# Optimization experiments

Measured on AMD Instinct MI355X. Metric: run time of the kernel, lower is better.

The kernel has to match this reference:

```python
import jax, jax.numpy as jnp
import numpy as np

C0 = 32          # cs[0] == cs[1] with planes=[32,32,...], cr=1.0
CIN = 4
EPS = 1e-5

# ---------- host-side coordinate hashing (mirrors F.sphash / F.sphashquery) ----------

def _enc(c):
    # unique int64 code per (x,y,z); +2 shift keeps offset-adjusted coords positive
    return (c[:, 0] + 2).astype(np.int64) + (c[:, 1] + 2).astype(np.int64) * 1024 \
        + (c[:, 2] + 2).astype(np.int64) * 1024 * 1024

def _lookup(sorted_codes, q):
    pos = np.searchsorted(sorted_codes, q)
    pos = np.minimum(pos, len(sorted_codes) - 1)
    return np.where(sorted_codes[pos] == q, pos, -1).astype(np.int32)

def _offsets(r):
    return np.array([[i, j, k] for i in r for j in r for k in r], np.int64)


def setup_inputs() -> dict:
    rng = np.random.default_rng(0)
    N0 = 400000
    pts = rng.integers(0, [400, 400, 40], size=(600000, 3)).astype(np.int64)
    codes = _enc(pts)
    codes_u, idx = np.unique(codes, return_index=True)
    assert len(codes_u) >= N0
    coords0, codes0 = pts[idx][:N0], codes_u[:N0]   # sorted by hash code

    off27, off8 = _offsets([-1, 0, 1]), _offsets([0, 1])
    # ks=3 stride=1 kernel map at level 0: nbr0[k, i] = index of coords0[i]+off27[k] (or -1)
    nbr0 = np.stack([_lookup(codes0, _enc(coords0 + o)) for o in off27])

    # stride-2 downsample coords (level 1)
    c1all = coords0 // 2
    codes1_u, i1 = np.unique(_enc(c1all), return_index=True)
    coords1 = c1all[i1]
    # ks=2 stride=2 kernel map: output voxel gathers inputs at 2*out + {0,1}^3
    down1 = np.stack([_lookup(codes0, _enc(coords1 * 2 + o)) for o in off8])
    # ks=3 stride=1 kernel map at level 1
    nbr1 = np.stack([_lookup(codes1_u, _enc(coords1 + o)) for o in off27])

    key = jax.random.key(0)
    ks = jax.random.split(key, 10)

    def w(k, K, ci, co):
        return jax.random.normal(k, (K, ci, co), jnp.float32) * (1.0 / np.sqrt(K * ci))

    return {
        "voxel_features": jax.random.normal(ks[0], (N0, CIN), jnp.float32),
        "W_stem1": w(ks[1], 27, CIN, C0),
        "W_stem2": w(ks[2], 27, C0, C0),
        "W_down":  w(ks[3], 8,  C0, C0),
        "W_r1a":   w(ks[4], 27, C0, C0),
        "W_r1b":   w(ks[5], 27, C0, C0),
        "W_r2a":   w(ks[6], 27, C0, C0),
        "W_r2b":   w(ks[7], 27, C0, C0),
        "gammas": jnp.ones((7, C0), jnp.float32),
        "betas":  jnp.zeros((7, C0), jnp.float32),
        "nbr0":  jnp.asarray(nbr0),
        "down1": jnp.asarray(down1),
        "nbr1":  jnp.asarray(nbr1),
    }


# ---------- sparse conv: gather-GEMM-scatter per kernel offset ----------

def _spconv(feat, nbr, W):
    # feat [N, Ci], nbr [K, M] (-1 = no neighbor), W [K, Ci, Co] -> out [M, Co]
    def step(acc, kw):
        idx, Wk = kw
        g = jnp.where((idx >= 0)[:, None], feat[jnp.maximum(idx, 0)], 0.0)
        return acc + g @ Wk, None
    acc0 = jnp.zeros((nbr.shape[1], W.shape[-1]), feat.dtype)
    out, _ = jax.lax.scan(step, acc0, (nbr, W))
    return out


def _bn(x, g, b):
    # BatchNorm1d, training-mode statistics (biased var), gamma/beta affine
    mu = x.mean(0)
    var = x.var(0)
    return (x - mu) * jax.lax.rsqrt(var + EPS) * g + b


def _cbr(x, nbr, W, g, b):
    return jax.nn.relu(_bn(_spconv(x, nbr, W), g, b))


def reference(voxel_features, W_stem1, W_stem2, W_down, W_r1a, W_r1b, W_r2a, W_r2b,
              gammas, betas, nbr0, down1, nbr1):
    g, b = gammas, betas
    # stem: two ks=3 sparse convs + BN + ReLU at level 0
    x = _cbr(voxel_features, nbr0, W_stem1, g[0], b[0])
    x = _cbr(x, nbr0, W_stem2, g[1], b[1])
    # stage1: BasicConvolutionBlock (ks=2, stride=2) + 2 ResidualBlocks at level 1
    x1 = _cbr(x, down1, W_down, g[2], b[2])
    h = _cbr(x1, nbr1, W_r1a, g[3], b[3])
    h = _bn(_spconv(h, nbr1, W_r1b), g[4], b[4])
    x1 = jax.nn.relu(h + x1)          # downsample == Identity (inc == outc, stride 1)
    h = _cbr(x1, nbr1, W_r2a, g[5], b[5])
    h = _bn(_spconv(h, nbr1, W_r2b), g[6], b[6])
    return jax.nn.relu(h + x1)
```

## Files before the change

kernel.cpp:

```cpp
#include <hip/hip_runtime.h>

#define EPS 1e-5f

typedef __attribute__((ext_vector_type(8))) short short8;
typedef __attribute__((ext_vector_type(4))) float floatx4;
typedef __attribute__((ext_vector_type(8))) unsigned short ushort8;
typedef __attribute__((ext_vector_type(4))) unsigned short ushortv4;

#define O_S1  0
#define O_S2  4096
#define O_DN  (O_S2 + 27648)
#define O_R1A (O_DN + 8192)
#define O_R1B (O_R1A + 27648)
#define O_R2A (O_R1B + 27648)
#define O_R2B (O_R2A + 27648)
#define WP_TOTAL (O_R2B + 27648)

__device__ __forceinline__ unsigned short f2bf(float f) {
    union { float f; unsigned u; } x; x.f = f;
    unsigned r = x.u + 0x7fffu + ((x.u >> 16) & 1u);
    return (unsigned short)(r >> 16);
}
__device__ __forceinline__ float bf2f(unsigned short b) {
    union { unsigned u; float f; } x; x.u = ((unsigned)b) << 16;
    return x.f;
}

__device__ __forceinline__ int xcd_swizzle(int nb) {
    int b = (int)blockIdx.x;
    int q = nb >> 3, r = nb & 7;
    int x = b & 7, i = b >> 3;
    return x * q + (x < r ? x : r) + i;
}

__device__ __forceinline__ void pack_w_one(
    const float* __restrict__ W, unsigned short* __restrict__ out, int t)
{
    int lane = t & 63;
    int h = (t >> 6) & 1;
    int k = t >> 7;
    int m = lane & 15, q = lane >> 4;
    ushort8 v;
#pragma unroll
    for (int j = 0; j < 8; ++j)
        v[j] = f2bf(W[((size_t)k * 32 + q * 8 + j) * 32 + h * 16 + m]);
    *(ushort8*)(out + (size_t)t * 8) = v;
}

__global__ __launch_bounds__(256) void prep_kernel(
    const float* __restrict__ vf,
    const float* __restrict__ Ws1, const float* __restrict__ Ws2,
    const float* __restrict__ Wd,  const float* __restrict__ Wr1a,
    const float* __restrict__ Wr1b, const float* __restrict__ Wr2a,
    const float* __restrict__ Wr2b,
    unsigned short* __restrict__ xb, unsigned short* __restrict__ wp, int N0)
{
    int t = blockIdx.x * 256 + threadIdx.x;
    if (t < N0) {
        float4 v = *(const float4*)(vf + (size_t)t * 4);
        ushortv4 r = {f2bf(v.x), f2bf(v.y), f2bf(v.z), f2bf(v.w)};
        *(ushortv4*)(xb + (size_t)t * 4) = r;
        return;
    }
    t -= N0;
    if (t < 512) {
        int lane = t & 63;
        int h = (t >> 6) & 1;
        int c = t >> 7;
        int m = lane & 15, q = lane >> 4;
        ushort8 v;
#pragma unroll
        for (int j = 0; j < 8; ++j) {
            int kdim = c * 32 + q * 8 + j;
            int tap = kdim >> 2, ci = kdim & 3;
            v[j] = (tap < 27) ? f2bf(Ws1[((size_t)tap * 4 + ci) * 32 + h * 16 + m]) : 0;
        }
        *(ushort8*)(wp + O_S1 + (size_t)t * 8) = v;
        return;
    }
    t -= 512;
    if (t < 27 * 128) { pack_w_one(Ws2,  wp + O_S2,  t); return; }
    t -= 27 * 128;
    if (t < 8 * 128)  { pack_w_one(Wd,   wp + O_DN,  t); return; }
    t -= 8 * 128;
    if (t < 27 * 128) { pack_w_one(Wr1a, wp + O_R1A, t); return; }
    t -= 27 * 128;
    if (t < 27 * 128) { pack_w_one(Wr1b, wp + O_R1B, t); return; }
    t -= 27 * 128;
    if (t < 27 * 128) { pack_w_one(Wr2a, wp + O_R2A, t); return; }
    t -= 27 * 128;
    if (t < 27 * 128) { pack_w_one(Wr2b, wp + O_R2B, t); return; }
}

__device__ __forceinline__ void conv_epilogue(
    floatx4 acc00, floatx4 acc01, floatx4 acc10, floatx4 acc11,
    unsigned short* __restrict__ y, float* __restrict__ part,
    int rowbase, int lb, int N, float* sm)
{
    const int lane = threadIdx.x & 63;
    const int m = lane & 15, q = lane >> 4;

    if (threadIdx.x < 64) sm[threadIdx.x] = 0.f;
    __syncthreads();

#pragma unroll
    for (int r = 0; r < 4; ++r) {
        int ra = rowbase + q * 4 + r;
        int rb = ra + 16;
        if (ra < N) {
            y[(size_t)ra * 32 + m]      = f2bf(acc00[r]);
            y[(size_t)ra * 32 + 16 + m] = f2bf(acc01[r]);
        }
        if (rb < N) {
            y[(size_t)rb * 32 + m]      = f2bf(acc10[r]);
            y[(size_t)rb * 32 + 16 + m] = f2bf(acc11[r]);
        }
    }

    float s0 = 0.f, q0 = 0.f, s1 = 0.f, q1 = 0.f;
#pragma unroll
    for (int r = 0; r < 4; ++r) {
        s0 += acc00[r] + acc10[r];
        q0 += acc00[r] * acc00[r] + acc10[r] * acc10[r];
        s1 += acc01[r] + acc11[r];
        q1 += acc01[r] * acc01[r] + acc11[r] * acc11[r];
    }
    s0 += __shfl_down(s0, 32); s0 += __shfl_down(s0, 16);
    q0 += __shfl_down(q0, 32); q0 += __shfl_down(q0, 16);
    s1 += __shfl_down(s1, 32); s1 += __shfl_down(s1, 16);
    q1 += __shfl_down(q1, 32); q1 += __shfl_down(q1, 16);
    if (lane < 16) {
        atomicAdd(&sm[m],      s0);
        atomicAdd(&sm[32 + m], q0);
        atomicAdd(&sm[16 + m],      s1);
        atomicAdd(&sm[48 + m], q1);
    }
    __syncthreads();
    if (threadIdx.x < 64)
        part[(size_t)lb * 64 + threadIdx.x] = sm[threadIdx.x];
}

template <int K>
__global__ __launch_bounds__(256) void conv_mfma_kernel(
    const unsigned short* __restrict__ x,
    const int* __restrict__ nbr,
    const unsigned short* __restrict__ Wp,
    unsigned short* __restrict__ y,
    float* __restrict__ part, int N)
{
    __shared__ float sm[64];
    const int nb = (N + 127) / 128;
    const int lb = xcd_swizzle(nb);
    const int lane = threadIdx.x & 63;
    const int wave = threadIdx.x >> 6;
    const int m = lane & 15, q = lane >> 4;
    const int rowbase = lb * 128 + wave * 32;
    const int row0 = rowbase + m;
    const int row1 = rowbase + 16 + m;

    floatx4 acc00 = {0.f, 0.f, 0.f, 0.f};
    floatx4 acc01 = acc00, acc10 = acc00, acc11 = acc00;

    for (int k = 0; k < K; ++k) {
        int i0 = (row0 < N) ? nbr[(size_t)k * N + row0] : -1;
        int i1 = (row1 < N) ? nbr[(size_t)k * N + row1] : -1;
        short8 a0 = {}, a1 = {};
        if (i0 >= 0) a0 = *(const short8*)(x + (size_t)i0 * 32 + q * 8);
        if (i1 >= 0) a1 = *(const short8*)(x + (size_t)i1 * 32 + q * 8);
        const short8* wk = (const short8*)(Wp + (size_t)k * 2 * 64 * 8);
        short8 b0 = wk[lane];
        short8 b1 = wk[64 + lane];
        acc00 = __builtin_amdgcn_mfma_f32_16x16x32_bf16(a0, b0, acc00, 0, 0, 0);
        acc01 = __builtin_amdgcn_mfma_f32_16x16x32_bf16(a0, b1, acc01, 0, 0, 0);
        acc10 = __builtin_amdgcn_mfma_f32_16x16x32_bf16(a1, b0, acc10, 0, 0, 0);
        acc11 = __builtin_amdgcn_mfma_f32_16x16x32_bf16(a1, b1, acc11, 0, 0, 0);
    }

    conv_epilogue(acc00, acc01, acc10, acc11, y, part, rowbase, lb, N, sm);
}

__global__ __launch_bounds__(256) void conv_stem1_mfma(
    const unsigned short* __restrict__ xb,
    const int* __restrict__ nbr,
    const unsigned short* __restrict__ Wp,
    unsigned short* __restrict__ y,
    float* __restrict__ part, int N)
{
    __shared__ float sm[64];
    const int nb = (N + 127) / 128;
    const int lb = xcd_swizzle(nb);
    const int lane = threadIdx.x & 63;
    const int wave = threadIdx.x >> 6;
    const int m = lane & 15, q = lane >> 4;
    const int rowbase = lb * 128 + wave * 32;
    const int row0 = rowbase + m;
    const int row1 = rowbase + 16 + m;

    floatx4 acc00 = {0.f, 0.f, 0.f, 0.f};
    floatx4 acc01 = acc00, acc10 = acc00, acc11 = acc00;

#pragma unroll
    for (int c = 0; c < 4; ++c) {
        const int t0 = c * 8 + q * 2, t1 = t0 + 1;
        short8 a0 = {}, a1 = {};
        {
            int ia = (t0 < 27 && row0 < N) ? nbr[(size_t)t0 * N + row0] : -1;
            int ib = (t1 < 27 && row0 < N) ? nbr[(size_t)t1 * N + row0] : -1;
            ushortv4 ga = {}, gb = {};
            if (ia >= 0) ga = *(const ushortv4*)(xb + (size_t)ia * 4);
            if (ib >= 0) gb = *(const ushortv4*)(xb + (size_t)ib * 4);
            a0[0] = (short)ga[0]; a0[1] = (short)ga[1];
            a0[2] = (short)ga[2]; a0[3] = (short)ga[3];
            a0[4] = (short)gb[0]; a0[5] = (short)gb[1];
            a0[6] = (short)gb[2]; a0[7] = (short)gb[3];
        }
        {
            int ia = (t0 < 27 && row1 < N) ? nbr[(size_t)t0 * N + row1] : -1;
            int ib = (t1 < 27 && row1 < N) ? nbr[(size_t)t1 * N + row1] : -1;
            ushortv4 ga = {}, gb = {};
            if (ia >= 0) ga = *(const ushortv4*)(xb + (size_t)ia * 4);
            if (ib >= 0) gb = *(const ushortv4*)(xb + (size_t)ib * 4);
            a1[0] = (short)ga[0]; a1[1] = (short)ga[1];
            a1[2] = (short)ga[2]; a1[3] = (short)ga[3];
            a1[4] = (short)gb[0]; a1[5] = (short)gb[1];
            a1[6] = (short)gb[2]; a1[7] = (short)gb[3];
        }
        const short8* wk = (const short8*)Wp;
        short8 b0 = wk[(c * 2 + 0) * 64 + lane];
        short8 b1 = wk[(c * 2 + 1) * 64 + lane];
        acc00 = __builtin_amdgcn_mfma_f32_16x16x32_bf16(a0, b0, acc00, 0, 0, 0);
        acc01 = __builtin_amdgcn_mfma_f32_16x16x32_bf16(a0, b1, acc01, 0, 0, 0);
        acc10 = __builtin_amdgcn_mfma_f32_16x16x32_bf16(a1, b0, acc10, 0, 0, 0);
        acc11 = __builtin_amdgcn_mfma_f32_16x16x32_bf16(a1, b1, acc11, 0, 0, 0);
    }

    conv_epilogue(acc00, acc01, acc10, acc11, y, part, rowbase, lb, N, sm);
}

__global__ __launch_bounds__(256) void reduce_stats_kernel(
    const float* __restrict__ part, float* __restrict__ stats, int nb)
{
    __shared__ float sm[256];
    int t = threadIdx.x;
    int c = t & 63, g = t >> 6;
    float s = 0.f;
    for (int b = blockIdx.x * 4 + g; b < nb; b += 256)
        s += part[(size_t)b * 64 + c];
    sm[t] = s;
    __syncthreads();
    if (t < 64)
        atomicAdd(&stats[t], sm[t] + sm[64 + t] + sm[128 + t] + sm[192 + t]);
}

template <bool OUT_F32, bool HAS_RES>
__global__ __launch_bounds__(256) void bn_relu_kernel(
    const unsigned short* __restrict__ y, const float* __restrict__ stats,
    const float* __restrict__ gamma, const float* __restrict__ beta,
    const unsigned short* __restrict__ resid, void* __restrict__ outp, int N)
{
    int t = blockIdx.x * 256 + threadIdx.x;
    if (t >= N) return;
    float inv_n = 1.0f / (float)N;
    const ushort8* yr = (const ushort8*)(y + (size_t)t * 32);

#pragma unroll
    for (int c = 0; c < 4; ++c) {
        ushort8 v = yr[c];
        ushort8 rv = {};
        if (HAS_RES) rv = ((const ushort8*)(resid + (size_t)t * 32))[c];
        float f0, f1, f2, f3, f4, f5, f6, f7;
#define BNJ(fj, j)                                                        \
        {                                                                 \
            int co = c * 8 + (j);                                         \
            float mu = stats[co] * inv_n;                                 \
            float var = stats[32 + co] * inv_n - mu * mu;                 \
            float sc = rsqrtf(var + EPS) * gamma[co];                     \
            fj = (bf2f(v[j]) - mu) * sc + beta[co];                       \
            if (HAS_RES) fj += bf2f(rv[j]);                               \
            fj = fmaxf(fj, 0.0f);                                         \
        }
        BNJ(f0, 0) BNJ(f1, 1) BNJ(f2, 2) BNJ(f3, 3)
        BNJ(f4, 4) BNJ(f5, 5) BNJ(f6, 6) BNJ(f7, 7)
#undef BNJ
        if (OUT_F32) {
            float* ob = (float*)outp + (size_t)t * 32 + c * 8;
            floatx4 u0 = {f0, f1, f2, f3}, u1 = {f4, f5, f6, f7};
            *(floatx4*)(ob) = u0;
            *(floatx4*)(ob + 4) = u1;
        } else {
            ushort8 o;
            o[0] = f2bf(f0); o[1] = f2bf(f1); o[2] = f2bf(f2); o[3] = f2bf(f3);
            o[4] = f2bf(f4); o[5] = f2bf(f5); o[6] = f2bf(f6); o[7] = f2bf(f7);
            ((ushort8*)((unsigned short*)outp + (size_t)t * 32))[c] = o;
        }
    }
}

extern "C" void kernel_launch(void* const* d_in, const int* in_sizes, int n_in,
                              void* d_out, int out_size, void* d_ws, size_t ws_size,
                              hipStream_t stream)
{
    const float* vf   = (const float*)d_in[0];
    const float* Ws1  = (const float*)d_in[1];
    const float* Ws2  = (const float*)d_in[2];
    const float* Wd   = (const float*)d_in[3];
    const float* Wr1a = (const float*)d_in[4];
    const float* Wr1b = (const float*)d_in[5];
    const float* Wr2a = (const float*)d_in[6];
    const float* Wr2b = (const float*)d_in[7];
    const float* gam  = (const float*)d_in[8];
    const float* bet  = (const float*)d_in[9];
    const int* nbr0   = (const int*)d_in[10];
    const int* down1  = (const int*)d_in[11];
    const int* nbr1   = (const int*)d_in[12];

    int N0 = in_sizes[0] / 4;
    int N1 = in_sizes[11] / 8;

    unsigned short* yraw = (unsigned short*)d_ws;
    unsigned short* actA = yraw + (size_t)N0 * 32;
    unsigned short* actB = actA + (size_t)N0 * 32;
    unsigned short* xb   = actB + (size_t)N0 * 32;
    unsigned short* wp   = xb + (size_t)N0 * 4;
    float* part  = (float*)(wp + WP_TOTAL);
    float* stats = part + (size_t)3200 * 64;

    hipMemsetAsync(stats, 0, 7 * 64 * sizeof(float), stream);

    auto g1 = [](int n) { return dim3((unsigned)((n + 255) / 256)); };
    auto gm = [](int n) { return dim3((unsigned)((n + 127) / 128)); };
    int nb0 = (N0 + 127) / 128, nb1 = (N1 + 127) / 128;

    int prep_threads = N0 + 512 + 128 * (27 * 5 + 8);
    prep_kernel<<<g1(prep_threads), 256, 0, stream>>>(
        vf, Ws1, Ws2, Wd, Wr1a, Wr1b, Wr2a, Wr2b, xb, wp, N0);

    conv_stem1_mfma<<<gm(N0), 256, 0, stream>>>(xb, nbr0, wp + O_S1, yraw, part, N0);
    reduce_stats_kernel<<<64, 256, 0, stream>>>(part, stats + 0 * 64, nb0);
    bn_relu_kernel<false, false><<<g1(N0), 256, 0, stream>>>(yraw, stats + 0 * 64, gam + 0, bet + 0, nullptr, actA, N0);
    conv_mfma_kernel<27><<<gm(N0), 256, 0, stream>>>(actA, nbr0, wp + O_S2, yraw, part, N0);
    reduce_stats_kernel<<<64, 256, 0, stream>>>(part, stats + 1 * 64, nb0);
    bn_relu_kernel<false, false><<<g1(N0), 256, 0, stream>>>(yraw, stats + 1 * 64, gam + 32, bet + 32, nullptr, actB, N0);
    conv_mfma_kernel<8><<<gm(N1), 256, 0, stream>>>(actB, down1, wp + O_DN, yraw, part, N1);
    reduce_stats_kernel<<<64, 256, 0, stream>>>(part, stats + 2 * 64, nb1);
    bn_relu_kernel<false, false><<<g1(N1), 256, 0, stream>>>(yraw, stats + 2 * 64, gam + 64, bet + 64, nullptr, actA, N1);
    conv_mfma_kernel<27><<<gm(N1), 256, 0, stream>>>(actA, nbr1, wp + O_R1A, yraw, part, N1);
    reduce_stats_kernel<<<64, 256, 0, stream>>>(part, stats + 3 * 64, nb1);
    bn_relu_kernel<false, false><<<g1(N1), 256, 0, stream>>>(yraw, stats + 3 * 64, gam + 96, bet + 96, nullptr, actB, N1);
    conv_mfma_kernel<27><<<gm(N1), 256, 0, stream>>>(actB, nbr1, wp + O_R1B, yraw, part, N1);
    reduce_stats_kernel<<<64, 256, 0, stream>>>(part, stats + 4 * 64, nb1);
    bn_relu_kernel<false, true><<<g1(N1), 256, 0, stream>>>(yraw, stats + 4 * 64, gam + 128, bet + 128, actA, actB, N1);
    conv_mfma_kernel<27><<<gm(N1), 256, 0, stream>>>(actB, nbr1, wp + O_R2A, yraw, part, N1);
    reduce_stats_kernel<<<64, 256, 0, stream>>>(part, stats + 5 * 64, nb1);
    bn_relu_kernel<false, false><<<g1(N1), 256, 0, stream>>>(yraw, stats + 5 * 64, gam + 160, bet + 160, nullptr, actA, N1);
    conv_mfma_kernel<27><<<gm(N1), 256, 0, stream>>>(actA, nbr1, wp + O_R2B, yraw, part, N1);
    reduce_stats_kernel<<<64, 256, 0, stream>>>(part, stats + 6 * 64, nb1);
    bn_relu_kernel<true, true><<<g1(N1), 256, 0, stream>>>(yraw, stats + 6 * 64, gam + 192, bet + 192, actB, d_out, N1);
}
```

Baseline: 632.7 us.

## Double rows per wave and software-pipeline neighbor gathers in sparse conv

The generic sparse conv kernel now handles 64 rows per wave (256 per block) with eight MFMA accumulators, so each weight fragment load is reused across twice as many rows. The k-loop is software-pipelined: neighbor indices are prefetched two offsets ahead and feature gathers one offset ahead, to hide gather latency behind the MFMAs. The grid for these convs is halved, while stem1 keeps its 128-row tiling with a separate grid and partial count. This raises register pressure and lowers the number of blocks, which may reduce occupancy.

```diff
diff --git a/kernel.cpp b/kernel.cpp
--- a/kernel.cpp
+++ b/kernel.cpp
@@ -31,6 +31,12 @@
     int q = nb >> 3, r = nb & 7;
     int x = b & 7, i = b >> 3;
     return x * q + (x < r ? x : r) + i;
+}
+
+__device__ __forceinline__ short8 gath(const unsigned short* __restrict__ x,
+                                       int ii, int q) {
+    short8 z = {};
+    return (ii >= 0) ? *(const short8*)(x + (size_t)ii * 32 + q * 8) : z;
 }
 
 __device__ __forceinline__ void pack_w_one(
@@ -92,7 +98,7 @@
     if (t < 27 * 128) { pack_w_one(Wr2b, wp + O_R2B, t); return; }
 }
 
-__device__ __forceinline__ void conv_epilogue(
+__device__ __forceinline__ void conv_epilogue2(
     floatx4 acc00, floatx4 acc01, floatx4 acc10, floatx4 acc11,
     unsigned short* __restrict__ y, float* __restrict__ part,
     int rowbase, int lb, int N, float* sm)
@@ -140,6 +146,7 @@
         part[(size_t)lb * 64 + threadIdx.x] = sm[threadIdx.x];
 }
 
+#define MFMA_BF16 __builtin_amdgcn_mfma_f32_16x16x32_bf16
 template <int K>
 __global__ __launch_bounds__(256) void conv_mfma_kernel(
     const unsigned short* __restrict__ x,
@@ -149,34 +156,89 @@
     float* __restrict__ part, int N)
 {
     __shared__ float sm[64];
-    const int nb = (N + 127) / 128;
+    const int nb = (N + 255) / 256;
     const int lb = xcd_swizzle(nb);
     const int lane = threadIdx.x & 63;
     const int wave = threadIdx.x >> 6;
     const int m = lane & 15, q = lane >> 4;
-    const int rowbase = lb * 128 + wave * 32;
-    const int row0 = rowbase + m;
-    const int row1 = rowbase + 16 + m;
-
-    floatx4 acc00 = {0.f, 0.f, 0.f, 0.f};
-    floatx4 acc01 = acc00, acc10 = acc00, acc11 = acc00;
+    const int rowbase = lb * 256 + wave * 64;
+    const int r0 = rowbase + m, r1 = r0 + 16, r2 = r0 + 32, r3 = r0 + 48;
+    const bool v0 = r0 < N, v1 = r1 < N, v2 = r2 < N, v3 = r3 < N;
+
+    floatx4 c00 = {0.f, 0.f, 0.f, 0.f};
+    floatx4 c01 = c00, c10 = c00, c11 = c00;
+    floatx4 c20 = c00, c21 = c00, c30 = c00, c31 = c00;
+
+#define IDX(k, rr, vv) ((vv) ? nbr[(size_t)(k) * N + (rr)] : -1)
+
+    int p0 = IDX(0, r0, v0), p1 = IDX(0, r1, v1), p2 = IDX(0, r2, v2), p3 = IDX(0, r3, v3);
+    short8 a0 = gath(x, p0, q), a1 = gath(x, p1, q), a2 = gath(x, p2, q), a3 = gath(x, p3, q);
+    int j0 = -1, j1 = -1, j2 = -1, j3 = -1;
+    if (K > 1) { j0 = IDX(1, r0, v0); j1 = IDX(1, r1, v1); j2 = IDX(1, r2, v2); j3 = IDX(1, r3, v3); }
 
     for (int k = 0; k < K; ++k) {
-        int i0 = (row0 < N) ? nbr[(size_t)k * N + row0] : -1;
-        int i1 = (row1 < N) ? nbr[(size_t)k * N + row1] : -1;
-        short8 a0 = {}, a1 = {};
-        if (i0 >= 0) a0 = *(const short8*)(x + (size_t)i0 * 32 + q * 8);
-        if (i1 >= 0) a1 = *(const short8*)(x + (size_t)i1 * 32 + q * 8);
-        const short8* wk = (const short8*)(Wp + (size_t)k * 2 * 64 * 8);
+        int n0 = -1, n1 = -1, n2 = -1, n3 = -1;
+        if (k + 2 < K) {
+            n0 = IDX(k + 2, r0, v0); n1 = IDX(k + 2, r1, v1);
+            n2 = IDX(k + 2, r2, v2); n3 = IDX(k + 2, r3, v3);
+        }
+        short8 t0 = {}, t1 = {}, t2 = {}, t3 = {};
+        if (k + 1 < K) {
+            t0 = gath(x, j0, q); t1 = gath(x, j1, q);
+            t2 = gath(x, j2, q); t3 = gath(x, j3, q);
+        }
+        const short8* wk = (const short8*)(Wp + (size_t)k * 1024);
         short8 b0 = wk[lane];
         short8 b1 = wk[64 + lane];
-        acc00 = __builtin_amdgcn_mfma_f32_16x16x32_bf16(a0, b0, acc00, 0, 0, 0);
-        acc01 = __builtin_amdgcn_mfma_f32_16x16x32_bf16(a0, b1, acc01, 0, 0, 0);
-        acc10 = __builtin_amdgcn_mfma_f32_16x16x32_bf16(a1, b0, acc10, 0, 0, 0);
-        acc11 = __builtin_amdgcn_mfma_f32_16x16x32_bf16(a1, b1, acc11, 0, 0, 0);
-    }
-
-    conv_epilogue(acc00, acc01, acc10, acc11, y, part, rowbase, lb, N, sm);
+        c00 = MFMA_BF16(a0, b0, c00, 0, 0, 0);
+        c01 = MFMA_BF16(a0, b1, c01, 0, 0, 0);
+        c10 = MFMA_BF16(a1, b0, c10, 0, 0, 0);
+        c11 = MFMA_BF16(a1, b1, c11, 0, 0, 0);
+        c20 = MFMA_BF16(a2, b0, c20, 0, 0, 0);
+        c21 = MFMA_BF16(a2, b1, c21, 0, 0, 0);
+        c30 = MFMA_BF16(a3, b0, c30, 0, 0, 0);
+        c31 = MFMA_BF16(a3, b1, c31, 0, 0, 0);
+        a0 = t0; a1 = t1; a2 = t2; a3 = t3;
+        j0 = n0; j1 = n1; j2 = n2; j3 = n3;
+    }
+#undef IDX
+
+    if (threadIdx.x < 64) sm[threadIdx.x] = 0.f;
+    __syncthreads();
+
+#define STORE2(cA, cB, tb)                                        \
+    _Pragma("unroll")                                             \
+    for (int r = 0; r < 4; ++r) {                                 \
+        int ra = rowbase + (tb) * 16 + q * 4 + r;                 \
+        if (ra < N) {                                             \
+            y[(size_t)ra * 32 + m]      = f2bf(cA[r]);            \
+            y[(size_t)ra * 32 + 16 + m] = f2bf(cB[r]);            \
+        }                                                         \
+    }
+    STORE2(c00, c01, 0) STORE2(c10, c11, 1) STORE2(c20, c21, 2) STORE2(c30, c31, 3)
+#undef STORE2
+
+    float s0 = 0.f, q0 = 0.f, s1 = 0.f, q1 = 0.f;
+#pragma unroll
+    for (int r = 0; r < 4; ++r) {
+        s0 += c00[r] + c10[r] + c20[r] + c30[r];
+        q0 += c00[r] * c00[r] + c10[r] * c10[r] + c20[r] * c20[r] + c30[r] * c30[r];
+        s1 += c01[r] + c11[r] + c21[r] + c31[r];
+        q1 += c01[r] * c01[r] + c11[r] * c11[r] + c21[r] * c21[r] + c31[r] * c31[r];
+    }
+    s0 += __shfl_down(s0, 32); s0 += __shfl_down(s0, 16);
+    q0 += __shfl_down(q0, 32); q0 += __shfl_down(q0, 16);
+    s1 += __shfl_down(s1, 32); s1 += __shfl_down(s1, 16);
+    q1 += __shfl_down(q1, 32); q1 += __shfl_down(q1, 16);
+    if (lane < 16) {
+        atomicAdd(&sm[m],      s0);
+        atomicAdd(&sm[32 + m], q0);
+        atomicAdd(&sm[16 + m],      s1);
+        atomicAdd(&sm[48 + m], q1);
+    }
+    __syncthreads();
+    if (threadIdx.x < 64)
+        part[(size_t)lb * 64 + threadIdx.x] = sm[threadIdx.x];
 }
 
 __global__ __launch_bounds__(256) void conv_stem1_mfma(
@@ -228,13 +290,13 @@
         const short8* wk = (const short8*)Wp;
         short8 b0 = wk[(c * 2 + 0) * 64 + lane];
         short8 b1 = wk[(c * 2 + 1) * 64 + lane];
-        acc00 = __builtin_amdgcn_mfma_f32_16x16x32_bf16(a0, b0, acc00, 0, 0, 0);
-        acc01 = __builtin_amdgcn_mfma_f32_16x16x32_bf16(a0, b1, acc01, 0, 0, 0);
-        acc10 = __builtin_amdgcn_mfma_f32_16x16x32_bf16(a1, b0, acc10, 0, 0, 0);
-        acc11 = __builtin_amdgcn_mfma_f32_16x16x32_bf16(a1, b1, acc11, 0, 0, 0);
-    }
-
-    conv_epilogue(acc00, acc01, acc10, acc11, y, part, rowbase, lb, N, sm);
+        acc00 = MFMA_BF16(a0, b0, acc00, 0, 0, 0);
+        acc01 = MFMA_BF16(a0, b1, acc01, 0, 0, 0);
+        acc10 = MFMA_BF16(a1, b0, acc10, 0, 0, 0);
+        acc11 = MFMA_BF16(a1, b1, acc11, 0, 0, 0);
+    }
+
+    conv_epilogue2(acc00, acc01, acc10, acc11, y, part, rowbase, lb, N, sm);
 }
 
 __global__ __launch_bounds__(256) void reduce_stats_kernel(
@@ -328,15 +390,18 @@
     hipMemsetAsync(stats, 0, 7 * 64 * sizeof(float), stream);
 
     auto g1 = [](int n) { return dim3((unsigned)((n + 255) / 256)); };
-    auto gm = [](int n) { return dim3((unsigned)((n + 127) / 128)); };
-    int nb0 = (N0 + 127) / 128, nb1 = (N1 + 127) / 128;
+    auto gm = [](int n) { return dim3((unsigned)((n + 255) / 256)); };
+    auto gs = [](int n) { return dim3((unsigned)((n + 127) / 128)); };
+    int nbs1 = (N0 + 127) / 128;
+    int nb0 = (N0 + 255) / 256;
+    int nb1 = (N1 + 255) / 256;
 
     int prep_threads = N0 + 512 + 128 * (27 * 5 + 8);
     prep_kernel<<<g1(prep_threads), 256, 0, stream>>>(
         vf, Ws1, Ws2, Wd, Wr1a, Wr1b, Wr2a, Wr2b, xb, wp, N0);
 
-    conv_stem1_mfma<<<gm(N0), 256, 0, stream>>>(xb, nbr0, wp + O_S1, yraw, part, N0);
-    reduce_stats_kernel<<<64, 256, 0, stream>>>(part, stats + 0 * 64, nb0);
+    conv_stem1_mfma<<<gs(N0), 256, 0, stream>>>(xb, nbr0, wp + O_S1, yraw, part, N0);
+    reduce_stats_kernel<<<64, 256, 0, stream>>>(part, stats + 0 * 64, nbs1);
     bn_relu_kernel<false, false><<<g1(N0), 256, 0, stream>>>(yraw, stats + 0 * 64, gam + 0, bet + 0, nullptr, actA, N0);
     conv_mfma_kernel<27><<<gm(N0), 256, 0, stream>>>(actA, nbr0, wp + O_S2, yraw, part, N0);
     reduce_stats_kernel<<<64, 256, 0, stream>>>(part, stats + 1 * 64, nb0);
```

New measurement: 634.7 us. No clear change (+0.3%).

## Stage contiguous neighbor windows in LDS for sparse conv gathers

Applied to the files above, without the earlier changes.

The gather-MFMA conv kernel now groups taps by z-offset (3 groups of 9 for the 27-tap case, 2 groups of 4 for the 8-tap case) and loads all neighbor indices for a group up front. A block-wide min/max reduction finds the span of input rows those indices touch. If the span fits in a 448-row window, that slice is copied into LDS with coalesced loads and the MFMA operands are read from LDS; otherwise it falls back to global gathers. This aims to replace scattered global row gathers with one contiguous copy, relying on the hash-sorted row order keeping neighbors close. In exchange it adds extra block barriers, atomics, about 36 KB of LDS per block that may limit occupancy, and higher register pressure from holding 18 indices at once.

```diff
diff --git a/kernel.cpp b/kernel.cpp
--- a/kernel.cpp
+++ b/kernel.cpp
@@ -1,6 +1,7 @@
 #include <hip/hip_runtime.h>
 
 #define EPS 1e-5f
+#define WROWS 448
 
 typedef __attribute__((ext_vector_type(8))) short short8;
 typedef __attribute__((ext_vector_type(4))) float floatx4;
@@ -31,6 +32,12 @@
     int q = nb >> 3, r = nb & 7;
     int x = b & 7, i = b >> 3;
     return x * q + (x < r ? x : r) + i;
+}
+
+__device__ __forceinline__ short8 gath(const unsigned short* __restrict__ x,
+                                       int ii, int q) {
+    short8 z = {};
+    return (ii >= 0) ? *(const short8*)(x + (size_t)ii * 32 + q * 8) : z;
 }
 
 __device__ __forceinline__ void pack_w_one(
@@ -92,7 +99,7 @@
     if (t < 27 * 128) { pack_w_one(Wr2b, wp + O_R2B, t); return; }
 }
 
-__device__ __forceinline__ void conv_epilogue(
+__device__ __forceinline__ void conv_epilogue2(
     floatx4 acc00, floatx4 acc01, floatx4 acc10, floatx4 acc11,
     unsigned short* __restrict__ y, float* __restrict__ part,
     int rowbase, int lb, int N, float* sm)
@@ -140,6 +147,8 @@
         part[(size_t)lb * 64 + threadIdx.x] = sm[threadIdx.x];
 }
 
+#define MFMA_BF16 __builtin_amdgcn_mfma_f32_16x16x32_bf16
+
 template <int K>
 __global__ __launch_bounds__(256) void conv_mfma_kernel(
     const unsigned short* __restrict__ x,
@@ -148,35 +157,112 @@
     unsigned short* __restrict__ y,
     float* __restrict__ part, int N)
 {
+    constexpr int ZG  = (K == 27) ? 3 : 2;
+    constexpr int TPG = (K == 27) ? 9 : 4;
+
+    __shared__ __align__(16) unsigned short win[WROWS * 40];
     __shared__ float sm[64];
+    __shared__ int wmm[2 * 3];
+
     const int nb = (N + 127) / 128;
     const int lb = xcd_swizzle(nb);
     const int lane = threadIdx.x & 63;
     const int wave = threadIdx.x >> 6;
     const int m = lane & 15, q = lane >> 4;
     const int rowbase = lb * 128 + wave * 32;
-    const int row0 = rowbase + m;
-    const int row1 = rowbase + 16 + m;
-
-    floatx4 acc00 = {0.f, 0.f, 0.f, 0.f};
-    floatx4 acc01 = acc00, acc10 = acc00, acc11 = acc00;
-
-    for (int k = 0; k < K; ++k) {
-        int i0 = (row0 < N) ? nbr[(size_t)k * N + row0] : -1;
-        int i1 = (row1 < N) ? nbr[(size_t)k * N + row1] : -1;
-        short8 a0 = {}, a1 = {};
-        if (i0 >= 0) a0 = *(const short8*)(x + (size_t)i0 * 32 + q * 8);
-        if (i1 >= 0) a1 = *(const short8*)(x + (size_t)i1 * 32 + q * 8);
-        const short8* wk = (const short8*)(Wp + (size_t)k * 2 * 64 * 8);
-        short8 b0 = wk[lane];
-        short8 b1 = wk[64 + lane];
-        acc00 = __builtin_amdgcn_mfma_f32_16x16x32_bf16(a0, b0, acc00, 0, 0, 0);
-        acc01 = __builtin_amdgcn_mfma_f32_16x16x32_bf16(a0, b1, acc01, 0, 0, 0);
-        acc10 = __builtin_amdgcn_mfma_f32_16x16x32_bf16(a1, b0, acc10, 0, 0, 0);
-        acc11 = __builtin_amdgcn_mfma_f32_16x16x32_bf16(a1, b1, acc11, 0, 0, 0);
-    }
-
-    conv_epilogue(acc00, acc01, acc10, acc11, y, part, rowbase, lb, N, sm);
+    const int r0 = rowbase + m;
+    const int r1 = r0 + 16;
+    const bool v0 = r0 < N, v1 = r1 < N;
+
+    floatx4 c00 = {0.f, 0.f, 0.f, 0.f};
+    floatx4 c01 = c00, c10 = c00, c11 = c00;
+
+    if (threadIdx.x < 2 * ZG)
+        wmm[threadIdx.x] = (threadIdx.x & 1) ? -1 : 0x7fffffff;
+    __syncthreads();
+
+#define IDX(k, rr, vv) ((vv) ? nbr[(size_t)(k) * N + (rr)] : -1)
+#define LG(ii) ({ short8 z_ = {}; \
+    (ii) >= 0 ? *(const short8*)(&win[((ii) - wmin) * 40 + q * 8]) : z_; })
+#define MN(a) ((a) < 0 ? 0x7fffffff : (a))
+
+    for (int c = 0; c < ZG; ++c) {
+        int ia0 = (0 < TPG) ? IDX(c + ZG * 0, r0, v0) : -1;
+        int ib0 = (0 < TPG) ? IDX(c + ZG * 0, r1, v1) : -1;
+        int ia1 = (1 < TPG) ? IDX(c + ZG * 1, r0, v0) : -1;
+        int ib1 = (1 < TPG) ? IDX(c + ZG * 1, r1, v1) : -1;
+        int ia2 = (2 < TPG) ? IDX(c + ZG * 2, r0, v0) : -1;
+        int ib2 = (2 < TPG) ? IDX(c + ZG * 2, r1, v1) : -1;
+        int ia3 = (3 < TPG) ? IDX(c + ZG * 3, r0, v0) : -1;
+        int ib3 = (3 < TPG) ? IDX(c + ZG * 3, r1, v1) : -1;
+        int ia4 = (4 < TPG) ? IDX(c + ZG * 4, r0, v0) : -1;
+        int ib4 = (4 < TPG) ? IDX(c + ZG * 4, r1, v1) : -1;
+        int ia5 = (5 < TPG) ? IDX(c + ZG * 5, r0, v0) : -1;
+        int ib5 = (5 < TPG) ? IDX(c + ZG * 5, r1, v1) : -1;
+        int ia6 = (6 < TPG) ? IDX(c + ZG * 6, r0, v0) : -1;
+        int ib6 = (6 < TPG) ? IDX(c + ZG * 6, r1, v1) : -1;
+        int ia7 = (7 < TPG) ? IDX(c + ZG * 7, r0, v0) : -1;
+        int ib7 = (7 < TPG) ? IDX(c + ZG * 7, r1, v1) : -1;
+        int ia8 = (8 < TPG) ? IDX(c + ZG * 8, r0, v0) : -1;
+        int ib8 = (8 < TPG) ? IDX(c + ZG * 8, r1, v1) : -1;
+
+        int lmin = min(min(min(min(MN(ia0), MN(ib0)), min(MN(ia1), MN(ib1))),
+                           min(min(MN(ia2), MN(ib2)), min(MN(ia3), MN(ib3)))),
+                       min(min(min(MN(ia4), MN(ib4)), min(MN(ia5), MN(ib5))),
+                           min(min(MN(ia6), MN(ib6)),
+                               min(min(MN(ia7), MN(ib7)), min(MN(ia8), MN(ib8))))));
+        int lmax = max(max(max(max(ia0, ib0), max(ia1, ib1)),
+                           max(max(ia2, ib2), max(ia3, ib3))),
+                       max(max(max(ia4, ib4), max(ia5, ib5)),
+                           max(max(ia6, ib6), max(max(ia7, ib7), max(ia8, ib8)))));
+#pragma unroll
+        for (int off = 32; off >= 1; off >>= 1) {
+            lmin = min(lmin, __shfl_down(lmin, off));
+            lmax = max(lmax, __shfl_down(lmax, off));
+        }
+        if (lane == 0) { atomicMin(&wmm[2 * c], lmin); atomicMax(&wmm[2 * c + 1], lmax); }
+        __syncthreads();
+
+        const int wmin = wmm[2 * c];
+        const int wmax = wmm[2 * c + 1];
+        const bool any = (wmax >= 0);
+        const int wspan = wmax - wmin + 1;
+        const bool use_lds = any && (wspan <= WROWS);
+
+        if (use_lds) {
+            const short8* src = (const short8*)(x + (size_t)wmin * 32);
+            for (int cc = threadIdx.x; cc < wspan * 4; cc += 256) {
+                int rr = cc >> 2, hh = cc & 3;
+                *(short8*)&win[rr * 40 + hh * 8] = src[cc];
+            }
+        }
+        __syncthreads();
+
+#define TAPC(J, iA, iB)                                                   \
+        if (J < TPG) {                                                    \
+            const short8* wk = (const short8*)(Wp + (size_t)(c + ZG * J) * 1024); \
+            short8 b0 = wk[lane];                                         \
+            short8 b1 = wk[64 + lane];                                    \
+            short8 a0, a1;                                                \
+            if (use_lds) { a0 = LG(iA); a1 = LG(iB); }                    \
+            else         { a0 = gath(x, iA, q); a1 = gath(x, iB, q); }    \
+            c00 = MFMA_BF16(a0, b0, c00, 0, 0, 0);                        \
+            c01 = MFMA_BF16(a0, b1, c01, 0, 0, 0);                        \
+            c10 = MFMA_BF16(a1, b0, c10, 0, 0, 0);                        \
+            c11 = MFMA_BF16(a1, b1, c11, 0, 0, 0);                        \
+        }
+        if (any) {
+            TAPC(0, ia0, ib0) TAPC(1, ia1, ib1) TAPC(2, ia2, ib2)
+            TAPC(3, ia3, ib3) TAPC(4, ia4, ib4) TAPC(5, ia5, ib5)
+            TAPC(6, ia6, ib6) TAPC(7, ia7, ib7) TAPC(8, ia8, ib8)
+        }
+#undef TAPC
+    }
+#undef IDX
+#undef LG
+#undef MN
+
+    conv_epilogue2(c00, c01, c10, c11, y, part, rowbase, lb, N, sm);
 }
 
 __global__ __launch_bounds__(256) void conv_stem1_mfma(
@@ -228,13 +314,13 @@
         const short8* wk = (const short8*)Wp;
         short8 b0 = wk[(c * 2 + 0) * 64 + lane];
         short8 b1 = wk[(c * 2 + 1) * 64 + lane];
-        acc00 = __builtin_amdgcn_mfma_f32_16x16x32_bf16(a0, b0, acc00, 0, 0, 0);
-        acc01 = __builtin_amdgcn_mfma_f32_16x16x32_bf16(a0, b1, acc01, 0, 0, 0);
-        acc10 = __builtin_amdgcn_mfma_f32_16x16x32_bf16(a1, b0, acc10, 0, 0, 0);
-        acc11 = __builtin_amdgcn_mfma_f32_16x16x32_bf16(a1, b1, acc11, 0, 0, 0);
-    }
-
-    conv_epilogue(acc00, acc01, acc10, acc11, y, part, rowbase, lb, N, sm);
+        acc00 = MFMA_BF16(a0, b0, acc00, 0, 0, 0);
+        acc01 = MFMA_BF16(a0, b1, acc01, 0, 0, 0);
+        acc10 = MFMA_BF16(a1, b0, acc10, 0, 0, 0);
+        acc11 = MFMA_BF16(a1, b1, acc11, 0, 0, 0);
+    }
+
+    conv_epilogue2(acc00, acc01, acc10, acc11, y, part, rowbase, lb, N, sm);
 }
 
 __global__ __launch_bounds__(256) void reduce_stats_kernel(
@@ -329,7 +415,8 @@
 
     auto g1 = [](int n) { return dim3((unsigned)((n + 255) / 256)); };
     auto gm = [](int n) { return dim3((unsigned)((n + 127) / 128)); };
-    int nb0 = (N0 + 127) / 128, nb1 = (N1 + 127) / 128;
+    int nb0 = (N0 + 127) / 128;
+    int nb1 = (N1 + 127) / 128;
 
     int prep_threads = N0 + 512 + 128 * (27 * 5 + 8);
     prep_kernel<<<g1(prep_threads), 256, 0, stream>>>(
```

New measurement: 632.0 us. No clear change (-0.1%).
